# Kernel optimization log

Hardware: AMD Instinct MI355X
Metric: run time of the kernel (lower is better)

## Reference

```python
import jax, jax.numpy as jnp
import numpy as np

B, H, N, D, M = 1, 4, 2048, 64, 256  # batch, heads, seq, dim_heads, nb_features
EPS = 1e-4


def _gaussian_orthogonal_random_matrix(nb_rows, nb_cols, seed=0):
    # scaling=1 path of the torch code: stacked transposed-Q orthogonal blocks,
    # scaled by sqrt(nb_cols).
    rng = np.random.default_rng(seed)
    blocks = []
    for _ in range(nb_rows // nb_cols):
        q, _ = np.linalg.qr(rng.standard_normal((nb_cols, nb_cols)))
        blocks.append(q.T)
    final = np.concatenate(blocks, axis=0)  # [nb_rows, nb_cols]
    return jnp.asarray(np.sqrt(float(nb_cols)) * final, dtype=jnp.float32)


def setup_inputs() -> dict:
    key = jax.random.key(0)
    kq, kk, kv = jax.random.split(key, 3)
    return {
        "q": jax.random.normal(kq, (B, H, N, D), dtype=jnp.float32),
        "k": jax.random.normal(kk, (B, H, N, D), dtype=jnp.float32),
        "v": jax.random.normal(kv, (B, H, N, D), dtype=jnp.float32),
        "projection_matrix": _gaussian_orthogonal_random_matrix(M, D),
    }


def _softmax_kernel(data, projection_matrix, is_query):
    # data: [B,H,N,D], projection_matrix: [M,D] -> features [B,H,N,M]
    data_normalizer = 1.0 / data.shape[-1] ** 0.25
    ratio = 1.0 / projection_matrix.shape[0] ** 0.5
    data_dash = jnp.einsum("bhnd,md->bhnm", data_normalizer * data, projection_matrix)
    diag_data = jnp.sum(data * data, axis=-1) * 0.5 * data_normalizer ** 2  # [B,H,N]
    diag_data = diag_data[..., None]  # [B,H,N,1]
    if is_query:
        stab = jnp.max(data_dash, axis=-1, keepdims=True)
    else:
        stab = jnp.max(data_dash)
    return ratio * (jnp.exp(data_dash - diag_data - stab) + EPS)


def _causal_linear_attention(q, k, v):
    # q,k: [B,H,N,M] features; v: [B,H,N,E]
    k_cumsum = jnp.cumsum(k, axis=-2)                       # [B,H,N,M]
    context = jnp.einsum("bhnm,bhne->bhnme", k, v)          # outer products
    context = jnp.cumsum(context, axis=-3)                  # cumulative over n
    context = context / k_cumsum[..., None]                 # [B,H,N,M,E]
    return jnp.einsum("bhnme,bhnm->bhne", context, q)


def reference(q, k, v, projection_matrix):
    q_feat = _softmax_kernel(q, projection_matrix, is_query=True)
    k_feat = _softmax_kernel(k, projection_matrix, is_query=False)
    return _causal_linear_attention(q_feat, k_feat, v)
```

## Files before the change

### kernel.cpp

```cpp
#include <hip/hip_runtime.h>
#include <math.h>

#define NH   4
#define SEQ  2048
#define DH   64
#define NF   256
#define ROWS (NH*SEQ)
#define DN    0.35355339059327373f
#define DIAGC 0.0625f
#define RATIO 0.0625f
#define EPSF  1e-4f

typedef __attribute__((ext_vector_type(8))) short bf8;
typedef __attribute__((ext_vector_type(4))) short bf4;
typedef __attribute__((ext_vector_type(4))) float f4;

static __device__ __forceinline__ unsigned short f2bf(float x) {
  union { float f; unsigned u; } v; v.f = x;
  unsigned r = v.u + 0x7FFF + ((v.u >> 16) & 1);
  return (unsigned short)(r >> 16);
}
static __device__ __forceinline__ float bf2f(unsigned short b) {
  union { unsigned u; float f; } v; v.u = ((unsigned)b) << 16;
  return v.f;
}

__global__ __launch_bounds__(256) void k_proj(const float* __restrict__ q,
    const float* __restrict__ k, const float* __restrict__ v,
    const float* __restrict__ P,
    unsigned short* __restrict__ qfb, float* __restrict__ dshd,
    float* __restrict__ bmax, unsigned short* __restrict__ vtb) {
  __shared__ float lds[64*65];
  const int b = blockIdx.x;
  if (b >= 512) {
    const int cb = b - 512;
    const int h = cb >> 5, n0 = (cb & 31) * 64;
    const int tid = threadIdx.x;
    for (int i = tid; i < 4096; i += 256) {
      int n = i >> 6, e = i & 63;
      lds[n*65 + e] = v[((size_t)h*SEQ + n0 + n)*DH + e];
    }
    __syncthreads();
    for (int i = tid; i < 4096; i += 256) {
      int e = i >> 6, n = i & 63;
      vtb[((size_t)h*DH + e)*SEQ + n0 + n] = f2bf(lds[n*65 + e]);
    }
    return;
  }
  const int tile = b;
  const int w = threadIdx.x >> 6, lane = threadIdx.x & 63;
  const int lr = lane & 15, g = lane >> 4;

  const float* xq = q + (size_t)tile*16*DH;
  const float* xk = k + (size_t)tile*16*DH;
  f4 qa = *(const f4*)(xq + lr*DH + g*8);
  f4 qb = *(const f4*)(xq + lr*DH + g*8 + 4);
  f4 qc = *(const f4*)(xq + lr*DH + 32 + g*8);
  f4 qd = *(const f4*)(xq + lr*DH + 32 + g*8 + 4);
  f4 ka = *(const f4*)(xk + lr*DH + g*8);
  f4 kb_ = *(const f4*)(xk + lr*DH + g*8 + 4);
  f4 kc = *(const f4*)(xk + lr*DH + 32 + g*8);
  f4 kd = *(const f4*)(xk + lr*DH + 32 + g*8 + 4);
  float ssq = 0.f, ssk = 0.f;
#pragma unroll
  for (int i = 0; i < 4; ++i) {
    ssq += qa[i]*qa[i] + qb[i]*qb[i] + qc[i]*qc[i] + qd[i]*qd[i];
    ssk += ka[i]*ka[i] + kb_[i]*kb_[i] + kc[i]*kc[i] + kd[i]*kd[i];
  }
  ssq += __shfl_xor(ssq, 16); ssq += __shfl_xor(ssq, 32);
  ssk += __shfl_xor(ssk, 16); ssk += __shfl_xor(ssk, 32);

  bf8 qh0, qh1, ql0, ql1, kh0, kh1, kl0, kl1;
#pragma unroll
  for (int i = 0; i < 4; ++i) {
    {
      float v0 = DN*qa[i], v1 = DN*qb[i], v2 = DN*qc[i], v3 = DN*qd[i];
      unsigned short h0 = f2bf(v0), h1 = f2bf(v1), h2 = f2bf(v2), h3 = f2bf(v3);
      qh0[i] = (short)h0; qh0[i+4] = (short)h1;
      qh1[i] = (short)h2; qh1[i+4] = (short)h3;
      ql0[i]   = (short)f2bf(v0 - bf2f(h0)); ql0[i+4] = (short)f2bf(v1 - bf2f(h1));
      ql1[i]   = (short)f2bf(v2 - bf2f(h2)); ql1[i+4] = (short)f2bf(v3 - bf2f(h3));
    }
    {
      float v0 = DN*ka[i], v1 = DN*kb_[i], v2 = DN*kc[i], v3 = DN*kd[i];
      unsigned short h0 = f2bf(v0), h1 = f2bf(v1), h2 = f2bf(v2), h3 = f2bf(v3);
      kh0[i] = (short)h0; kh0[i+4] = (short)h1;
      kh1[i] = (short)h2; kh1[i+4] = (short)h3;
      kl0[i]   = (short)f2bf(v0 - bf2f(h0)); kl0[i+4] = (short)f2bf(v1 - bf2f(h1));
      kl1[i]   = (short)f2bf(v2 - bf2f(h2)); kl1[i+4] = (short)f2bf(v3 - bf2f(h3));
    }
  }

  const int ct0 = w*4;
  f4 dshq[4], dshk[4];
#pragma unroll
  for (int cc = 0; cc < 4; ++cc) {
    const int ct = ct0 + cc;
    const float* prow = P + (ct*16 + lr)*DH + g*8;
    f4 p0 = *(const f4*)(prow);
    f4 p1 = *(const f4*)(prow + 4);
    f4 p2 = *(const f4*)(prow + 32);
    f4 p3 = *(const f4*)(prow + 36);
    bf8 bh0, bl0, bh1, bl1;
#pragma unroll
    for (int i = 0; i < 4; ++i) {
      unsigned short h0 = f2bf(p0[i]), h1 = f2bf(p1[i]);
      unsigned short h2 = f2bf(p2[i]), h3 = f2bf(p3[i]);
      bh0[i] = (short)h0; bh0[i+4] = (short)h1;
      bh1[i] = (short)h2; bh1[i+4] = (short)h3;
      bl0[i]   = (short)f2bf(p0[i] - bf2f(h0)); bl0[i+4] = (short)f2bf(p1[i] - bf2f(h1));
      bl1[i]   = (short)f2bf(p2[i] - bf2f(h2)); bl1[i+4] = (short)f2bf(p3[i] - bf2f(h3));
    }
    f4 aq = {0.f, 0.f, 0.f, 0.f};
    aq = __builtin_amdgcn_mfma_f32_16x16x32_bf16(qh0, bh0, aq, 0, 0, 0);
    aq = __builtin_amdgcn_mfma_f32_16x16x32_bf16(qh1, bh1, aq, 0, 0, 0);
    aq = __builtin_amdgcn_mfma_f32_16x16x32_bf16(qh0, bl0, aq, 0, 0, 0);
    aq = __builtin_amdgcn_mfma_f32_16x16x32_bf16(qh1, bl1, aq, 0, 0, 0);
    aq = __builtin_amdgcn_mfma_f32_16x16x32_bf16(ql0, bh0, aq, 0, 0, 0);
    aq = __builtin_amdgcn_mfma_f32_16x16x32_bf16(ql1, bh1, aq, 0, 0, 0);
    dshq[cc] = aq;
    f4 ak = {0.f, 0.f, 0.f, 0.f};
    ak = __builtin_amdgcn_mfma_f32_16x16x32_bf16(kh0, bh0, ak, 0, 0, 0);
    ak = __builtin_amdgcn_mfma_f32_16x16x32_bf16(kh1, bh1, ak, 0, 0, 0);
    ak = __builtin_amdgcn_mfma_f32_16x16x32_bf16(kh0, bl0, ak, 0, 0, 0);
    ak = __builtin_amdgcn_mfma_f32_16x16x32_bf16(kh1, bl1, ak, 0, 0, 0);
    ak = __builtin_amdgcn_mfma_f32_16x16x32_bf16(kl0, bh0, ak, 0, 0, 0);
    ak = __builtin_amdgcn_mfma_f32_16x16x32_bf16(kl1, bh1, ak, 0, 0, 0);
    dshk[cc] = ak;
  }

  f4 mrq, mrk;
#pragma unroll
  for (int r = 0; r < 4; ++r) {
    mrq[r] = fmaxf(fmaxf(dshq[0][r], dshq[1][r]), fmaxf(dshq[2][r], dshq[3][r]));
    mrk[r] = fmaxf(fmaxf(dshk[0][r], dshk[1][r]), fmaxf(dshk[2][r], dshk[3][r]));
  }
#pragma unroll
  for (int mk = 1; mk <= 8; mk <<= 1) {
#pragma unroll
    for (int r = 0; r < 4; ++r) {
      mrq[r] = fmaxf(mrq[r], __shfl_xor(mrq[r], mk));
      mrk[r] = fmaxf(mrk[r], __shfl_xor(mrk[r], mk));
    }
  }
  if (lr == 0) {
#pragma unroll
    for (int r = 0; r < 4; ++r) {
      lds[w*16 + 4*g + r]      = mrq[r];
      lds[64 + w*16 + 4*g + r] = mrk[r];
    }
  }
  __syncthreads();
  float rmq[4], rmk[4], srq[4], srk[4];
#pragma unroll
  for (int r = 0; r < 4; ++r) {
    rmq[r] = fmaxf(fmaxf(lds[0*16 + 4*g + r], lds[1*16 + 4*g + r]),
                   fmaxf(lds[2*16 + 4*g + r], lds[3*16 + 4*g + r]));
    rmk[r] = fmaxf(fmaxf(lds[64 + 0*16 + 4*g + r], lds[64 + 1*16 + 4*g + r]),
                   fmaxf(lds[64 + 2*16 + 4*g + r], lds[64 + 3*16 + 4*g + r]));
    srq[r] = __shfl(ssq, 4*g + r);
    srk[r] = __shfl(ssk, 4*g + r);
  }

  {
    unsigned short* ob = qfb + (size_t)tile*16*NF;
#pragma unroll
    for (int cc = 0; cc < 4; ++cc) {
#pragma unroll
      for (int r = 0; r < 4; ++r)
        ob[(4*g + r)*NF + (ct0 + cc)*16 + lr] =
            f2bf(RATIO*(expf(dshq[cc][r] - (srq[r]*DIAGC + rmq[r])) + EPSF));
    }
  }
  {
    float* db = dshd + (size_t)tile*16*NF;
#pragma unroll
    for (int cc = 0; cc < 4; ++cc) {
#pragma unroll
      for (int r = 0; r < 4; ++r)
        db[(4*g + r)*NF + (ct0 + cc)*16 + lr] = dshk[cc][r] - srk[r]*DIAGC;
    }
    float tmax = fmaxf(fmaxf(rmk[0], rmk[1]), fmaxf(rmk[2], rmk[3]));
    tmax = fmaxf(tmax, __shfl_xor(tmax, 16));
    tmax = fmaxf(tmax, __shfl_xor(tmax, 32));
    if (w == 0 && lane == 0) bmax[tile] = tmax;
  }
}

__global__ __launch_bounds__(256) void k_feat2(const float* __restrict__ dshd,
    const float* __restrict__ bmax, unsigned short* __restrict__ kfb,
    unsigned short* __restrict__ kft, float* __restrict__ csum) {
  const int u = blockIdx.x, m = threadIdx.x;
  const int h = u >> 7, t = u & 127;
  __shared__ float red[256];
  red[m] = fmaxf(bmax[m], bmax[m + 256]);
  __syncthreads();
  for (int s = 128; s > 0; s >>= 1) {
    if (m < s) red[m] = fmaxf(red[m], red[m+s]);
    __syncthreads();
  }
  const float gg = red[0];
  const float* db = dshd + (size_t)u*16*NF + m;
  unsigned short* ob = kfb + (size_t)u*16*NF + m;
  float run = 0.f;
  bf8 k0, k1;
#pragma unroll
  for (int r = 0; r < 16; ++r) {
    unsigned short bv = f2bf(RATIO*(expf(db[r*NF] - gg) + EPSF));
    ob[r*NF] = bv;
    if (r < 8) k0[r] = (short)bv; else k1[r-8] = (short)bv;
    run += bf2f(bv);
  }
  csum[(size_t)u*NF + m] = run;
  unsigned short* kt = kft + ((size_t)(h*NF + m))*SEQ + t*16;
  *(bf8*)kt = k0;
  *(bf8*)(kt + 8) = k1;
}

__global__ __launch_bounds__(128) void k_state(
    const unsigned short* __restrict__ vtb, const unsigned short* __restrict__ kft,
    unsigned short* __restrict__ sthi, unsigned short* __restrict__ stlo,
    float* __restrict__ csum) {
  const int bx = blockIdx.x;
  if (bx >= 256) {
    if (threadIdx.x >= 64) return;
    const int h = bx - 256;
    const int m0 = threadIdx.x * 4;
    f4 run = {0.f, 0.f, 0.f, 0.f};
#pragma unroll 4
    for (int c = 0; c < 128; ++c) {
      float* p = csum + ((size_t)(h*128 + c))*NF + m0;
      f4 x = *(const f4*)p;
      *(f4*)p = run;
      run += x;
    }
    return;
  }
  __shared__ f4 bridge[64];
  const int wid = threadIdx.x >> 6, lane = threadIdx.x & 63;
  const int lr = lane & 15, g = lane >> 4;
  const int h = bx >> 6, et = (bx >> 4) & 3, mt = bx & 15;

  const unsigned short* vb = vtb + ((size_t)(h*DH + et*16 + lr))*SEQ;
  const unsigned short* kb = kft + ((size_t)(h*NF + mt*16 + lr))*SEQ;

  f4 cum = {0.f, 0.f, 0.f, 0.f};
  f4 loc[8];
  const int c0 = wid*8;
#pragma unroll
  for (int cc = 0; cc < 8; ++cc) {
    const int c = c0 + cc;
    if (wid == 0) {
      const size_t base = ((size_t)((h*16 + c)*64 + et*16 + 4*g))*NF + mt*16 + lr;
#pragma unroll
      for (int r = 0; r < 4; ++r) {
        unsigned short hi = f2bf(cum[r]);
        sthi[base + (size_t)r*NF] = hi;
        stlo[base + (size_t)r*NF] = f2bf(cum[r] - bf2f(hi));
      }
    } else {
      loc[cc] = cum;
    }
#pragma unroll
    for (int ks = 0; ks < 4; ++ks) {
      const int j0 = c*128 + ks*32 + g*8;
      bf8 xv = *(const bf8*)(vb + j0);
      bf8 ym = *(const bf8*)(kb + j0);
      cum = __builtin_amdgcn_mfma_f32_16x16x32_bf16(xv, ym, cum, 0, 0, 0);
    }
  }
  if (wid == 0) bridge[lane] = cum;
  __syncthreads();
  if (wid == 1) {
    f4 s8 = bridge[lane];
#pragma unroll
    for (int cc = 0; cc < 8; ++cc) {
      const int c = 8 + cc;
      f4 val = s8 + loc[cc];
      const size_t base = ((size_t)((h*16 + c)*64 + et*16 + 4*g))*NF + mt*16 + lr;
#pragma unroll
      for (int r = 0; r < 4; ++r) {
        unsigned short hi = f2bf(val[r]);
        sthi[base + (size_t)r*NF] = hi;
        stlo[base + (size_t)r*NF] = f2bf(val[r] - bf2f(hi));
      }
    }
  }
}

__global__ __launch_bounds__(128) void k_attn5(const unsigned short* __restrict__ qpb,
                                               const unsigned short* __restrict__ kfb,
                                               const unsigned short* __restrict__ vtb,
                                               const unsigned short* __restrict__ sthi,
                                               const unsigned short* __restrict__ stlo,
                                               const float* __restrict__ csum,
                                               float* __restrict__ out) {
  const int h = blockIdx.y;
  const int t = blockIdx.x;
  const int c = t >> 3;
  const int jc0 = c*8;
  const int nstage = (t & 7) + 1;
  const int tid = threadIdx.x;
  const int wid = tid >> 6, lane = tid & 63;
  const int lr = lane & 15, g = lane >> 4;

  __shared__ __align__(16) char smem[22528];
  char* Ks = smem + 8192;
  char* Vs = smem + 16384;
  float* MG = (float*)(smem + 18432);

  {
    const int u = h*128 + t;
    const int m = tid*2;
    float run0 = csum[(size_t)u*NF + m];
    float run1 = csum[(size_t)u*NF + m + 1];
    const unsigned short* kfp = kfb + ((size_t)(h*SEQ + t*16))*NF + m;
    const unsigned short* qfp = qpb + ((size_t)(h*SEQ + t*16))*NF + m;
#pragma unroll
    for (int r = 0; r < 16; ++r) {
      unsigned kv = *(const unsigned*)(kfp + (size_t)r*NF);
      unsigned qv = *(const unsigned*)(qfp + (size_t)r*NF);
      run0 += bf2f((unsigned short)(kv & 0xffff));
      run1 += bf2f((unsigned short)(kv >> 16));
      unsigned short q0 = f2bf(bf2f((unsigned short)(qv & 0xffff)) / run0);
      unsigned short q1 = f2bf(bf2f((unsigned short)(qv >> 16)) / run1);
      const int byte = (r*512 + m*2) ^ ((r & 7) << 4);
      *(unsigned*)(smem + byte) = (unsigned)q0 | ((unsigned)q1 << 16);
    }
  }
  __syncthreads();

  bf8 qf[8];
#pragma unroll
  for (int kb = 0; kb < 8; ++kb) {
    const int byte = (lr*512 + g*16 + kb*64) ^ ((lr & 7) << 4);
    qf[kb] = *(const bf8*)(smem + byte);
  }

  f4 o0 = {0,0,0,0}, o1 = {0,0,0,0}, o2 = {0,0,0,0}, o3 = {0,0,0,0};

  if (wid == 1) {
    const char* kTile = (const char*)(kfb + (size_t)h*SEQ*NF);
    const char* vTile = (const char*)(vtb + (size_t)h*DH*SEQ);
    int kw[8];
#pragma unroll
    for (int i = 0; i < 8; ++i) {
      const int ko = i*1024 + lane*16;
      kw[i] = ko ^ (((ko >> 9) & 7) << 4);
    }
    f4 sk[8], sv0, sv1;
    {
      const char* kt = kTile + (size_t)jc0*8192;
#pragma unroll
      for (int i = 0; i < 8; ++i) sk[i] = *(const f4*)(kt + i*1024 + lane*16);
      const char* vt = vTile + (size_t)lane*4096 + (size_t)jc0*32;
      sv0 = *(const f4*)(vt);
      sv1 = *(const f4*)(vt + 16);
    }
    for (int jj = 0; jj < nstage; ++jj) {
      const int j = jc0 + jj;
#pragma unroll
      for (int i = 0; i < 8; ++i) *(f4*)(Ks + kw[i]) = sk[i];
      *(f4*)(Vs + lane*32) = sv0;
      *(f4*)(Vs + lane*32 + 16) = sv1;
      if (jj + 1 < nstage) {
        const char* kt = kTile + (size_t)(j+1)*8192;
#pragma unroll
        for (int i = 0; i < 8; ++i) sk[i] = *(const f4*)(kt + i*1024 + lane*16);
        const char* vt = vTile + (size_t)lane*4096 + (size_t)(j+1)*32;
        sv0 = *(const f4*)(vt);
        sv1 = *(const f4*)(vt + 16);
      }
      bf8 kcs[8];
#pragma unroll
      for (int kb = 0; kb < 8; ++kb) {
        int off = (lr*512 + kb*64 + g*16) ^ ((lr & 7) << 4);
        kcs[kb] = *(const bf8*)(Ks + off);
      }
      f4 st = {0,0,0,0};
#pragma unroll
      for (int kb = 0; kb < 8; ++kb)
        st = __builtin_amdgcn_mfma_f32_16x16x32_bf16(kcs[kb], qf[kb], st, 0, 0, 0);
      if (j == t) {
#pragma unroll
        for (int rr = 0; rr < 4; ++rr) if (g*4 + rr > lr) st[rr] = 0.f;
      }
      bf8 sb = { (short)f2bf(st[0]), (short)f2bf(st[1]), (short)f2bf(st[2]), (short)f2bf(st[3]),
                 (short)0, (short)0, (short)0, (short)0 };
#pragma unroll
      for (int eb = 0; eb < 4; ++eb) {
        bf4 v4 = *(const bf4*)(Vs + (eb*16 + lr)*32 + g*8);
        bf8 vf = { v4[0], v4[1], v4[2], v4[3], (short)0, (short)0, (short)0, (short)0 };
        f4 acc = (eb == 0) ? o0 : (eb == 1) ? o1 : (eb == 2) ? o2 : o3;
        acc = __builtin_amdgcn_mfma_f32_16x16x32_bf16(sb, vf, acc, 0, 0, 0);
        if (eb == 0) o0 = acc; else if (eb == 1) o1 = acc; else if (eb == 2) o2 = acc; else o3 = acc;
      }
    }
    *(f4*)(MG + (0*64 + lane)*4) = o0;
    *(f4*)(MG + (1*64 + lane)*4) = o1;
    *(f4*)(MG + (2*64 + lane)*4) = o2;
    *(f4*)(MG + (3*64 + lane)*4) = o3;
  } else {
    const unsigned short* SH = sthi + ((size_t)((h*16 + c)*64 + lr))*NF + g*8;
    const unsigned short* SL = stlo + ((size_t)((h*16 + c)*64 + lr))*NF + g*8;
#pragma unroll
    for (int ks = 0; ks < 8; ++ks) {
#pragma unroll
      for (int et = 0; et < 4; ++et) {
        bf8 bh = *(const bf8*)(SH + et*16*NF + ks*32);
        bf8 bl = *(const bf8*)(SL + et*16*NF + ks*32);
        f4 acc = (et == 0) ? o0 : (et == 1) ? o1 : (et == 2) ? o2 : o3;
        acc = __builtin_amdgcn_mfma_f32_16x16x32_bf16(qf[ks], bh, acc, 0, 0, 0);
        acc = __builtin_amdgcn_mfma_f32_16x16x32_bf16(qf[ks], bl, acc, 0, 0, 0);
        if (et == 0) o0 = acc; else if (et == 1) o1 = acc; else if (et == 2) o2 = acc; else o3 = acc;
      }
    }
  }
  __syncthreads();

  if (wid == 0) {
    o0 += *(const f4*)(MG + (0*64 + lane)*4);
    o1 += *(const f4*)(MG + (1*64 + lane)*4);
    o2 += *(const f4*)(MG + (2*64 + lane)*4);
    o3 += *(const f4*)(MG + (3*64 + lane)*4);
    float* ob = out + ((size_t)(h*SEQ + t*16))*DH;
#pragma unroll
    for (int rr = 0; rr < 4; ++rr) {
      ob[(size_t)(4*g + rr)*DH +  0 + lr] = o0[rr];
      ob[(size_t)(4*g + rr)*DH + 16 + lr] = o1[rr];
      ob[(size_t)(4*g + rr)*DH + 32 + lr] = o2[rr];
      ob[(size_t)(4*g + rr)*DH + 48 + lr] = o3[rr];
    }
  }
}

extern "C" void kernel_launch(void* const* d_in, const int* in_sizes, int n_in,
                              void* d_out, int out_size, void* d_ws, size_t ws_size,
                              hipStream_t stream) {
  const float* q = (const float*)d_in[0];
  const float* k = (const float*)d_in[1];
  const float* v = (const float*)d_in[2];
  const float* P = (const float*)d_in[3];
  float* out = (float*)d_out;

  char* ws = (char*)d_ws;
  unsigned short* qfb  = (unsigned short*)(ws);
  unsigned short* kfb  = (unsigned short*)(ws + (4u<<20));
  unsigned short* vtb  = (unsigned short*)(ws + (8u<<20));
  unsigned short* kft  = (unsigned short*)(ws + (12u<<20));
  float* dshd   = (float*)(ws + (16u<<20));
  float* bmax   = (float*)(ws + (24u<<20));
  float* csum   = (float*)(ws + (25u<<20));
  unsigned short* sthi = (unsigned short*)(ws + (33u<<20));
  unsigned short* stlo = (unsigned short*)(ws + (36u<<20));

  k_proj  <<<640, 256, 0, stream>>>(q, k, v, P, qfb, dshd, bmax, vtb);
  k_feat2 <<<512, 256, 0, stream>>>(dshd, bmax, kfb, kft, csum);
  k_state <<<260, 128, 0, stream>>>(vtb, kft, sthi, stlo, csum);
  k_attn5 <<<dim3(128, NH), 128, 0, stream>>>(qfb, kfb, vtb, sthi, stlo, csum, out);
}
```

Measured before the change: 49.72 us.

## Split projection and intra-chunk attention work across more wavefronts

The projection kernel now runs 512 threads per block, so each of 8 waves handles 2 feature tiles instead of 4, and the row-max reduction is widened to 8 partials. The attention kernel adds a third wave: two waves alternate over the intra-chunk key/value stages with separate LDS buffers and partial-sum slots, which wave 0 then adds in. The goal is more parallelism and latency hiding per block. In exchange it uses more LDS and more registers per block, and the projection kernel recomputes P conversions in more waves.

```diff
diff --git a/kernel.cpp b/kernel.cpp
--- a/kernel.cpp
+++ b/kernel.cpp
@@ -25,7 +25,7 @@
   return v.f;
 }
 
-__global__ __launch_bounds__(256) void k_proj(const float* __restrict__ q,
+__global__ __launch_bounds__(512) void k_proj(const float* __restrict__ q,
     const float* __restrict__ k, const float* __restrict__ v,
     const float* __restrict__ P,
     unsigned short* __restrict__ qfb, float* __restrict__ dshd,
@@ -36,12 +36,12 @@
     const int cb = b - 512;
     const int h = cb >> 5, n0 = (cb & 31) * 64;
     const int tid = threadIdx.x;
-    for (int i = tid; i < 4096; i += 256) {
+    for (int i = tid; i < 4096; i += 512) {
       int n = i >> 6, e = i & 63;
       lds[n*65 + e] = v[((size_t)h*SEQ + n0 + n)*DH + e];
     }
     __syncthreads();
-    for (int i = tid; i < 4096; i += 256) {
+    for (int i = tid; i < 4096; i += 512) {
       int e = i >> 6, n = i & 63;
       vtb[((size_t)h*DH + e)*SEQ + n0 + n] = f2bf(lds[n*65 + e]);
     }
@@ -91,10 +91,10 @@
     }
   }
 
-  const int ct0 = w*4;
-  f4 dshq[4], dshk[4];
-#pragma unroll
-  for (int cc = 0; cc < 4; ++cc) {
+  const int ct0 = w*2;
+  f4 dshq[2], dshk[2];
+#pragma unroll
+  for (int cc = 0; cc < 2; ++cc) {
     const int ct = ct0 + cc;
     const float* prow = P + (ct*16 + lr)*DH + g*8;
     f4 p0 = *(const f4*)(prow);
@@ -132,8 +132,8 @@
   f4 mrq, mrk;
 #pragma unroll
   for (int r = 0; r < 4; ++r) {
-    mrq[r] = fmaxf(fmaxf(dshq[0][r], dshq[1][r]), fmaxf(dshq[2][r], dshq[3][r]));
-    mrk[r] = fmaxf(fmaxf(dshk[0][r], dshk[1][r]), fmaxf(dshk[2][r], dshk[3][r]));
+    mrq[r] = fmaxf(dshq[0][r], dshq[1][r]);
+    mrk[r] = fmaxf(dshk[0][r], dshk[1][r]);
   }
 #pragma unroll
   for (int mk = 1; mk <= 8; mk <<= 1) {
@@ -146,18 +146,21 @@
   if (lr == 0) {
 #pragma unroll
     for (int r = 0; r < 4; ++r) {
-      lds[w*16 + 4*g + r]      = mrq[r];
-      lds[64 + w*16 + 4*g + r] = mrk[r];
+      lds[w*16 + 4*g + r]       = mrq[r];
+      lds[128 + w*16 + 4*g + r] = mrk[r];
     }
   }
   __syncthreads();
   float rmq[4], rmk[4], srq[4], srk[4];
 #pragma unroll
   for (int r = 0; r < 4; ++r) {
-    rmq[r] = fmaxf(fmaxf(lds[0*16 + 4*g + r], lds[1*16 + 4*g + r]),
-                   fmaxf(lds[2*16 + 4*g + r], lds[3*16 + 4*g + r]));
-    rmk[r] = fmaxf(fmaxf(lds[64 + 0*16 + 4*g + r], lds[64 + 1*16 + 4*g + r]),
-                   fmaxf(lds[64 + 2*16 + 4*g + r], lds[64 + 3*16 + 4*g + r]));
+    float mq = lds[0*16 + 4*g + r], mk2 = lds[128 + 0*16 + 4*g + r];
+#pragma unroll
+    for (int w2 = 1; w2 < 8; ++w2) {
+      mq  = fmaxf(mq,  lds[w2*16 + 4*g + r]);
+      mk2 = fmaxf(mk2, lds[128 + w2*16 + 4*g + r]);
+    }
+    rmq[r] = mq; rmk[r] = mk2;
     srq[r] = __shfl(ssq, 4*g + r);
     srk[r] = __shfl(ssk, 4*g + r);
   }
@@ -165,7 +168,7 @@
   {
     unsigned short* ob = qfb + (size_t)tile*16*NF;
 #pragma unroll
-    for (int cc = 0; cc < 4; ++cc) {
+    for (int cc = 0; cc < 2; ++cc) {
 #pragma unroll
       for (int r = 0; r < 4; ++r)
         ob[(4*g + r)*NF + (ct0 + cc)*16 + lr] =
@@ -175,7 +178,7 @@
   {
     float* db = dshd + (size_t)tile*16*NF;
 #pragma unroll
-    for (int cc = 0; cc < 4; ++cc) {
+    for (int cc = 0; cc < 2; ++cc) {
 #pragma unroll
       for (int r = 0; r < 4; ++r)
         db[(4*g + r)*NF + (ct0 + cc)*16 + lr] = dshk[cc][r] - srk[r]*DIAGC;
@@ -288,7 +291,7 @@
   }
 }
 
-__global__ __launch_bounds__(128) void k_attn5(const unsigned short* __restrict__ qpb,
+__global__ __launch_bounds__(192) void k_attn6(const unsigned short* __restrict__ qpb,
                                                const unsigned short* __restrict__ kfb,
                                                const unsigned short* __restrict__ vtb,
                                                const unsigned short* __restrict__ sthi,
@@ -304,12 +307,15 @@
   const int wid = tid >> 6, lane = tid & 63;
   const int lr = lane & 15, g = lane >> 4;
 
-  __shared__ __align__(16) char smem[22528];
-  char* Ks = smem + 8192;
-  char* Vs = smem + 16384;
-  float* MG = (float*)(smem + 18432);
-
-  {
+  __shared__ __align__(16) char smem[36864];
+  char* Ks1 = smem + 8192;
+  char* Vs1 = smem + 16384;
+  char* Ks2 = smem + 18432;
+  char* Vs2 = smem + 26624;
+  float* MG1 = (float*)(smem + 28672);
+  float* MG2 = (float*)(smem + 32768);
+
+  if (tid < 128) {
     const int u = h*128 + t;
     const int m = tid*2;
     float run0 = csum[(size_t)u*NF + m];
@@ -339,7 +345,9 @@
 
   f4 o0 = {0,0,0,0}, o1 = {0,0,0,0}, o2 = {0,0,0,0}, o3 = {0,0,0,0};
 
-  if (wid == 1) {
+  if (wid >= 1) {
+    char* Ks = (wid == 1) ? Ks1 : Ks2;
+    char* Vs = (wid == 1) ? Vs1 : Vs2;
     const char* kTile = (const char*)(kfb + (size_t)h*SEQ*NF);
     const char* vTile = (const char*)(vtb + (size_t)h*DH*SEQ);
     int kw[8];
@@ -349,25 +357,26 @@
       kw[i] = ko ^ (((ko >> 9) & 7) << 4);
     }
     f4 sk[8], sv0, sv1;
-    {
-      const char* kt = kTile + (size_t)jc0*8192;
+    int jj = wid - 1;
+    if (jj < nstage) {
+      const char* kt = kTile + (size_t)(jc0 + jj)*8192;
 #pragma unroll
       for (int i = 0; i < 8; ++i) sk[i] = *(const f4*)(kt + i*1024 + lane*16);
-      const char* vt = vTile + (size_t)lane*4096 + (size_t)jc0*32;
+      const char* vt = vTile + (size_t)lane*4096 + (size_t)(jc0 + jj)*32;
       sv0 = *(const f4*)(vt);
       sv1 = *(const f4*)(vt + 16);
     }
-    for (int jj = 0; jj < nstage; ++jj) {
+    for (; jj < nstage; jj += 2) {
       const int j = jc0 + jj;
 #pragma unroll
       for (int i = 0; i < 8; ++i) *(f4*)(Ks + kw[i]) = sk[i];
       *(f4*)(Vs + lane*32) = sv0;
       *(f4*)(Vs + lane*32 + 16) = sv1;
-      if (jj + 1 < nstage) {
-        const char* kt = kTile + (size_t)(j+1)*8192;
+      if (jj + 2 < nstage) {
+        const char* kt = kTile + (size_t)(j + 2)*8192;
 #pragma unroll
         for (int i = 0; i < 8; ++i) sk[i] = *(const f4*)(kt + i*1024 + lane*16);
-        const char* vt = vTile + (size_t)lane*4096 + (size_t)(j+1)*32;
+        const char* vt = vTile + (size_t)lane*4096 + (size_t)(j + 2)*32;
         sv0 = *(const f4*)(vt);
         sv1 = *(const f4*)(vt + 16);
       }
@@ -396,6 +405,7 @@
         if (eb == 0) o0 = acc; else if (eb == 1) o1 = acc; else if (eb == 2) o2 = acc; else o3 = acc;
       }
     }
+    float* MG = (wid == 1) ? MG1 : MG2;
     *(f4*)(MG + (0*64 + lane)*4) = o0;
     *(f4*)(MG + (1*64 + lane)*4) = o1;
     *(f4*)(MG + (2*64 + lane)*4) = o2;
@@ -419,10 +429,10 @@
   __syncthreads();
 
   if (wid == 0) {
-    o0 += *(const f4*)(MG + (0*64 + lane)*4);
-    o1 += *(const f4*)(MG + (1*64 + lane)*4);
-    o2 += *(const f4*)(MG + (2*64 + lane)*4);
-    o3 += *(const f4*)(MG + (3*64 + lane)*4);
+    o0 += *(const f4*)(MG1 + (0*64 + lane)*4) + *(const f4*)(MG2 + (0*64 + lane)*4);
+    o1 += *(const f4*)(MG1 + (1*64 + lane)*4) + *(const f4*)(MG2 + (1*64 + lane)*4);
+    o2 += *(const f4*)(MG1 + (2*64 + lane)*4) + *(const f4*)(MG2 + (2*64 + lane)*4);
+    o3 += *(const f4*)(MG1 + (3*64 + lane)*4) + *(const f4*)(MG2 + (3*64 + lane)*4);
     float* ob = out + ((size_t)(h*SEQ + t*16))*DH;
 #pragma unroll
     for (int rr = 0; rr < 4; ++rr) {
@@ -454,8 +464,8 @@
   unsigned short* sthi = (unsigned short*)(ws + (33u<<20));
   unsigned short* stlo = (unsigned short*)(ws + (36u<<20));
 
-  k_proj  <<<640, 256, 0, stream>>>(q, k, v, P, qfb, dshd, bmax, vtb);
+  k_proj  <<<640, 512, 0, stream>>>(q, k, v, P, qfb, dshd, bmax, vtb);
   k_feat2 <<<512, 256, 0, stream>>>(dshd, bmax, kfb, kft, csum);
   k_state <<<260, 128, 0, stream>>>(vtb, kft, sthi, stlo, csum);
-  k_attn5 <<<dim3(128, NH), 128, 0, stream>>>(qfb, kfb, vtb, sthi, stlo, csum, out);
-}
+  k_attn6 <<<dim3(128, NH), 192, 0, stream>>>(qfb, kfb, vtb, sthi, stlo, csum, out);
+}
```

Result: slower. 51.37 us (+3.3%).
